# Optimization experiments

Measured on AMD Instinct MI355X. Metric: run time of the kernel, lower is better.

The kernel has to match this reference:

```python
import jax, jax.numpy as jnp
import numpy as np

NEG_INF = -1e30  # masked_softmax fill (squad util convention)


def setup_inputs() -> dict:
    key = jax.random.key(0)
    ks = jax.random.split(key, 5)
    B, S, H = 4, 2048, 512
    x = jax.random.normal(ks[0], (B, S, H), dtype=jnp.float32)
    mask = jax.random.randint(ks[1], (B, S), 0, 2, dtype=jnp.int32)
    mask = mask.at[:, 0].set(1)  # ensure at least one valid key per row
    W_comb = jax.random.normal(ks[2], (H, 3 * H), dtype=jnp.float32) * (1.0 / np.sqrt(H))
    b_comb = jnp.zeros((3 * H,), dtype=jnp.float32)
    W_out = jax.random.normal(ks[3], (H, H), dtype=jnp.float32) * (1.0 / np.sqrt(H))
    b_out = jnp.zeros((H,), dtype=jnp.float32)
    return {"x": x, "mask": mask, "W_comb": W_comb, "b_comb": b_comb,
            "W_out": W_out, "b_out": b_out}


def reference(x, mask, W_comb, b_comb, W_out, b_out):
    B, S, H = x.shape
    n_head = 8
    d = H // n_head
    scale = d ** 0.5
    qkv = x @ W_comb + b_comb                      # [B,S,3H]
    q, k, v = jnp.split(qkv, 3, axis=-1)
    q = q.reshape(B, S, n_head, d)
    k = k.reshape(B, S, n_head, d)
    v = v.reshape(B, S, n_head, d)
    # [B,h,Sq,Sk] scores; mask applies along the key axis
    scores = jnp.einsum('bqhd,bkhd->bhqk', q / scale, k)
    key_mask = (mask > 0)[:, None, None, :]        # [B,1,1,Sk]
    logits = jnp.where(key_mask, scores, NEG_INF)
    attn = jax.nn.softmax(logits, axis=-1)         # dropout = identity (eval)
    out = jnp.einsum('bhqk,bkhd->bqhd', attn, v).reshape(B, S, H)
    return out @ W_out + b_out
```

## Files before the change

kernel.cpp:

```cpp
#include <hip/hip_runtime.h>
#include <hip/hip_bf16.h>
#include <stdint.h>

typedef unsigned short u16;
typedef __attribute__((ext_vector_type(8))) __bf16 bf16x8;
typedef __attribute__((ext_vector_type(8))) unsigned short us8;
typedef __attribute__((ext_vector_type(4))) unsigned short us4;
typedef __attribute__((ext_vector_type(4))) float f32x4;
typedef __attribute__((ext_vector_type(16))) float f32x16;

#define KSCALE_Q 0.18033688011112042f

__device__ inline u16 f2bf(float f) {
  union { __bf16 b; u16 s; } x; x.b = (__bf16)f; return x.s;
}
__device__ inline f32x16 zero16() {
  f32x16 z; for (int i = 0; i < 16; ++i) z[i] = 0.f; return z;
}
__device__ __forceinline__ void gl_lds16(const u16* g, u16* l) {
  __builtin_amdgcn_global_load_lds(
      (const __attribute__((address_space(1))) void*)g,
      (__attribute__((address_space(3))) void*)l, 16, 0, 0);
}

__global__ __launch_bounds__(256) void prep(
    const float* __restrict__ x, const float* __restrict__ Wc,
    const float* __restrict__ Wo, const int* __restrict__ mask,
    u16* __restrict__ xbf, u16* __restrict__ wct, u16* __restrict__ wot,
    int* __restrict__ idx, int* __restrict__ nbv) {
  int r = blockIdx.x, tid = threadIdx.x;
  if (r < 4096) {
    int i = r * 256 + tid;
    float4 v = ((const float4*)x)[i];
    us4 o;
    o[0] = f2bf(v.x); o[1] = f2bf(v.y); o[2] = f2bf(v.z); o[3] = f2bf(v.w);
    ((us4*)xbf)[i] = o;
    return;
  }
  __shared__ float tile[32][33];
  __shared__ int ps[256];
  if (r < 5120) {
    const float* in; u16* outT; int R, C, bi;
    if (r < 4864) { in = Wc; outT = wct; R = 512; C = 1536; bi = r - 4096; }
    else          { in = Wo; outT = wot; R = 512; C = 512;  bi = r - 4864; }
    int nbx = C >> 5;
    int bx = bi % nbx, by = bi / nbx;
    int xq = tid & 31, yq = tid >> 5;
    int c0 = bx * 32, r0 = by * 32;
    for (int j = 0; j < 32; j += 8)
      tile[yq + j][xq] = in[(size_t)(r0 + yq + j) * C + c0 + xq];
    __syncthreads();
    for (int j = 0; j < 32; j += 8)
      outT[(size_t)(c0 + yq + j) * R + r0 + xq] = f2bf(tile[xq][yq + j]);
    return;
  }
  int b = r - 5120;
  const int* mrow = mask + b * 2048;
  int4 a = ((const int4*)mrow)[tid * 2];
  int4 c = ((const int4*)mrow)[tid * 2 + 1];
  int v[8] = {a.x, a.y, a.z, a.w, c.x, c.y, c.z, c.w};
  int cnt = 0;
  for (int i = 0; i < 8; ++i) cnt += (v[i] > 0);
  ps[tid] = cnt;
  __syncthreads();
  for (int off = 1; off < 256; off <<= 1) {
    int xv = ps[tid];
    int yv = (tid >= off) ? ps[tid - off] : 0;
    __syncthreads();
    ps[tid] = xv + yv;
    __syncthreads();
  }
  int total = ps[255];
  int pos = ps[tid] - cnt;
  int* ip = idx + b * 2048;
  for (int i = 0; i < 8; ++i)
    if (v[i] > 0) ip[pos++] = tid * 8 + i;
  for (int i = 0; i < 8; ++i) {
    int j = tid * 8 + i;
    if (j >= total) ip[j] = 0;
  }
  if (tid == 0) nbv[b] = total;
}

template <int OB>
__global__ __launch_bounds__(256) void gemm64(
    const u16* __restrict__ A, const u16* __restrict__ Bt,
    const float* __restrict__ bias, void* __restrict__ Cout,
    int N, int K, float oscale) {
  int m0 = blockIdx.y * 128, n0 = blockIdx.x * 64;
  __shared__ __align__(16) u16 As[128 * 32];
  __shared__ __align__(16) u16 Bs[64 * 32];
  int tid = threadIdx.x, wave = tid >> 6, lane = tid & 63;
  int quad = lane >> 4, l16 = lane & 15;
  int wm = (wave >> 1) * 64, wn = (wave & 1) * 32;

  int arow0 = wave * 32 + (lane >> 2);
  int acb = (lane & 3) ^ ((lane >> 3) & 3);
  const u16* ag0 = A + (size_t)(m0 + arow0) * K + acb * 8;
  const u16* ag1 = ag0 + (size_t)16 * K;
  u16* al0 = As + wave * 32 * 32;
  u16* al1 = al0 + 16 * 32;
  int brow = wave * 16 + (lane >> 2);
  const u16* bg = Bt + (size_t)(n0 + brow) * K + acb * 8;
  u16* bl = Bs + wave * 16 * 32;

  f32x4 acc[4][2];
  for (int i = 0; i < 4; ++i)
    for (int j = 0; j < 2; ++j) acc[i][j] = (f32x4){0.f, 0.f, 0.f, 0.f};

  int swz = (l16 >> 1) & 3;
  for (int kk = 0; kk < K; kk += 32) {
    __syncthreads();
    gl_lds16(ag0 + kk, al0);
    gl_lds16(ag1 + kk, al1);
    gl_lds16(bg + kk, bl);
    __syncthreads();
    bf16x8 af[4], bfr[2];
    for (int i = 0; i < 4; ++i)
      af[i] = *(const bf16x8*)(As + (wm + i * 16 + l16) * 32 +
                               (quad ^ swz) * 8);
    for (int j = 0; j < 2; ++j)
      bfr[j] = *(const bf16x8*)(Bs + (wn + j * 16 + l16) * 32 +
                                (quad ^ swz) * 8);
    for (int i = 0; i < 4; ++i)
      for (int j = 0; j < 2; ++j)
        acc[i][j] = __builtin_amdgcn_mfma_f32_16x16x32_bf16(
            af[i], bfr[j], acc[i][j], 0, 0, 0);
  }
  for (int j = 0; j < 2; ++j) {
    int col = n0 + wn + j * 16 + l16;
    float bv = bias[col];
    for (int i = 0; i < 4; ++i) {
      int rowb = m0 + wm + i * 16 + quad * 4;
      for (int rr = 0; rr < 4; ++rr) {
        float v = (acc[i][j][rr] + bv) * oscale;
        if (OB)
          ((u16*)Cout)[(size_t)(rowb + rr) * N + col] = f2bf(v);
        else
          ((float*)Cout)[(size_t)(rowb + rr) * N + col] = v;
      }
    }
  }
}

__global__ __launch_bounds__(256) void gemm_kv(
    const u16* __restrict__ A, const u16* __restrict__ Bt,
    const float* __restrict__ bias, u16* __restrict__ Kc,
    u16* __restrict__ VTc, const int* __restrict__ idx,
    const int* __restrict__ nbv) {
  const int K = 512, N = 1024;
  int b = blockIdx.z;
  int m0 = blockIdx.y * 128, n0 = blockIdx.x * 64;
  int npad = (nbv[b] + 127) & ~127;
  if (m0 >= npad) return;
  __shared__ __align__(16) u16 As[128 * 32];
  __shared__ __align__(16) u16 Bs[64 * 32];
  int tid = threadIdx.x, wave = tid >> 6, lane = tid & 63;
  int quad = lane >> 4, l16 = lane & 15;
  int wm = (wave >> 1) * 64, wn = (wave & 1) * 32;

  int arow0 = wave * 32 + (lane >> 2);
  int acb = (lane & 3) ^ ((lane >> 3) & 3);
  int g0 = idx[b * 2048 + m0 + arow0];
  int g1 = idx[b * 2048 + m0 + arow0 + 16];
  const u16* ag0 = A + ((size_t)(b * 2048 + g0)) * K + acb * 8;
  const u16* ag1 = A + ((size_t)(b * 2048 + g1)) * K + acb * 8;
  u16* al0 = As + wave * 32 * 32;
  u16* al1 = al0 + 16 * 32;
  int brow = wave * 16 + (lane >> 2);
  const u16* bg = Bt + (size_t)(n0 + brow) * K + acb * 8;
  u16* bl = Bs + wave * 16 * 32;

  f32x4 acc[4][2];
  for (int i = 0; i < 4; ++i)
    for (int j = 0; j < 2; ++j) acc[i][j] = (f32x4){0.f, 0.f, 0.f, 0.f};

  int swz = (l16 >> 1) & 3;
  for (int kk = 0; kk < K; kk += 32) {
    __syncthreads();
    gl_lds16(ag0 + kk, al0);
    gl_lds16(ag1 + kk, al1);
    gl_lds16(bg + kk, bl);
    __syncthreads();
    bf16x8 af[4], bfr[2];
    for (int i = 0; i < 4; ++i)
      af[i] = *(const bf16x8*)(As + (wm + i * 16 + l16) * 32 +
                               (quad ^ swz) * 8);
    for (int j = 0; j < 2; ++j)
      bfr[j] = *(const bf16x8*)(Bs + (wn + j * 16 + l16) * 32 +
                                (quad ^ swz) * 8);
    for (int i = 0; i < 4; ++i)
      for (int j = 0; j < 2; ++j)
        acc[i][j] = __builtin_amdgcn_mfma_f32_16x16x32_bf16(
            af[i], bfr[j], acc[i][j], 0, 0, 0);
  }
  for (int j = 0; j < 2; ++j) {
    int col = n0 + wn + j * 16 + l16;
    float bv = bias[col];
    if (col < 512) {
      for (int i = 0; i < 4; ++i) {
        int key0 = m0 + wm + i * 16 + quad * 4;
        for (int rr = 0; rr < 4; ++rr)
          Kc[((size_t)b * 2048 + key0 + rr) * 512 + col] =
              f2bf(acc[i][j][rr] + bv);
      }
    } else {
      int hd = col - 512;
      int h = hd >> 6, d = hd & 63;
      u16* vrow = VTc + ((size_t)(b * 8 + h) * 64 + d) * 2048;
      for (int i = 0; i < 4; ++i) {
        int key0 = m0 + wm + i * 16 + quad * 4;
        us4 pk;
        for (int rr = 0; rr < 4; ++rr) pk[rr] = f2bf(acc[i][j][rr] + bv);
        *(us4*)(vrow + key0) = pk;
      }
    }
  }
}

__global__ __launch_bounds__(256) void attn_kernel(
    const u16* __restrict__ Qc, const u16* __restrict__ Kc,
    const u16* __restrict__ VTc, const int* __restrict__ nbv,
    u16* __restrict__ aout) {
  int b = blockIdx.z, h = blockIdx.y, q0 = blockIdx.x * 128;
  int bh = b * 8 + h;
  int tid = threadIdx.x, wave = tid >> 6, lane = tid & 63;
  int l5 = lane & 31, hi = lane >> 5;
  int nb = nbv[b];
  int npad = (nb + 127) & ~127;

  __shared__ __align__(16) u16 Kt[128 * 64];
  __shared__ __align__(16) u16 Vt[64 * 128];
  __shared__ __align__(16) u16 Pw[4][32 * 136];

  int qrow = b * 2048 + q0 + wave * 32 + l5;
  bf16x8 qf[4];
  for (int s = 0; s < 4; ++s)
    qf[s] = *(const bf16x8*)(Qc + (size_t)qrow * 512 + h * 64 + s * 16 + hi * 8);

  f32x16 o[2];
  o[0] = zero16(); o[1] = zero16();
  float lsum = 0.f;

  int krr = lane >> 3;
  int kcb = (lane & 7) ^ krr;
  const u16* kg = Kc + ((size_t)(b * 2048) + wave * 32 + krr) * 512 + h * 64 +
                  kcb * 8;
  u16* kl = Kt + (wave * 32) * 64 + lane * 8;
  int vrr = lane >> 4;
  const u16* vg = VTc + ((size_t)(bh * 64) + wave * 16 + vrr) * 2048;
  u16* vl = Vt + (wave * 16) * 128 + lane * 8;

  u16* pw = &Pw[wave][0] + l5 * 136;

  for (int kt0 = 0; kt0 < npad; kt0 += 128) {
    __syncthreads();
    for (int i = 0; i < 4; ++i)
      gl_lds16(kg + (size_t)(kt0 + i * 8) * 512, kl + i * 8 * 64);
    for (int i = 0; i < 4; ++i) {
      int vcb = (lane & 15) ^ ((i * 4 + vrr) & 7);
      gl_lds16(vg + (size_t)(i * 4) * 2048 + kt0 + vcb * 8, vl + i * 4 * 128);
    }
    __syncthreads();

    for (int kg4 = 0; kg4 < 4; ++kg4) {
      int krow = kg4 * 32 + l5;
      const u16* kro = Kt + krow * 64;
      int rx = krow & 7;
      f32x16 sa = zero16();
      for (int s = 0; s < 4; ++s) {
        bf16x8 ka = *(const bf16x8*)(kro + ((s * 2 + hi) ^ rx) * 8);
        sa = __builtin_amdgcn_mfma_f32_32x32x16_bf16(ka, qf[s], sa, 0, 0, 0);
      }
      if (kt0 + 128 > nb) {
        for (int r = 0; r < 16; ++r) {
          int jg = kt0 + kg4 * 32 + (r & 3) + 8 * (r >> 2) + 4 * hi;
          if (jg >= nb) sa[r] = -1e30f;
        }
      }
      for (int mI = 0; mI < 4; ++mI) {
        us4 pk;
        for (int r = 0; r < 4; ++r) {
          float e = exp2f(sa[mI * 4 + r]);
          lsum += e;
          pk[r] = f2bf(e);
        }
        *(us4*)(pw + kg4 * 32 + mI * 8 + hi * 4) = pk;
      }
    }

    for (int kh = 0; kh < 2; ++kh)
      for (int t = 0; t < 4; ++t) {
        bf16x8 pb = *(const bf16x8*)(pw + kh * 64 + t * 16 + hi * 8);
        for (int dc = 0; dc < 2; ++dc) {
          int vrow = dc * 32 + l5;
          bf16x8 va = *(const bf16x8*)(
              Vt + vrow * 128 + ((kh * 8 + t * 2 + hi) ^ (vrow & 7)) * 8);
          o[dc] = __builtin_amdgcn_mfma_f32_32x32x16_bf16(va, pb, o[dc], 0, 0, 0);
        }
      }
  }

  lsum += __shfl_xor(lsum, 32);
  float inv = 1.f / lsum;
  for (int dc = 0; dc < 2; ++dc)
    for (int mI = 0; mI < 4; ++mI) {
      us4 pk;
      for (int r = 0; r < 4; ++r) pk[r] = f2bf(o[dc][mI * 4 + r] * inv);
      *(us4*)(aout + (size_t)qrow * 512 + h * 64 + dc * 32 + mI * 8 + hi * 4) =
          pk;
    }
}

extern "C" void kernel_launch(void* const* d_in, const int* in_sizes, int n_in,
                              void* d_out, int out_size, void* d_ws,
                              size_t ws_size, hipStream_t stream) {
  const float* x = (const float*)d_in[0];
  const int* mask = (const int*)d_in[1];
  const float* Wc = (const float*)d_in[2];
  const float* bc = (const float*)d_in[3];
  const float* Wo = (const float*)d_in[4];
  const float* bo = (const float*)d_in[5];
  float* out = (float*)d_out;

  char* ws = (char*)d_ws;
  u16* xbf = (u16*)(ws);
  u16* wct = (u16*)(ws + 8388608);
  u16* wot = (u16*)(ws + 9961472);
  u16* Qc  = (u16*)(ws + 10485760);
  u16* Kc  = (u16*)(ws + 18874368);
  u16* vtc = (u16*)(ws + 27262976);
  int* idx = (int*)(ws + 35651584);
  int* nbv = (int*)(ws + 35684352);
  u16* aout = xbf;

  prep<<<5124, 256, 0, stream>>>(x, Wc, Wo, mask, xbf, wct, wot, idx, nbv);
  gemm64<1><<<dim3(8, 64), 256, 0, stream>>>(
      xbf, wct, bc, Qc, 512, 512, KSCALE_Q);
  gemm_kv<<<dim3(16, 16, 4), 256, 0, stream>>>(
      xbf, wct + (size_t)512 * 512, bc + 512, Kc, vtc, idx, nbv);
  attn_kernel<<<dim3(16, 8, 4), 256, 0, stream>>>(Qc, Kc, vtc, nbv, aout);
  gemm64<0><<<dim3(8, 64), 256, 0, stream>>>(
      aout, wot, bo, out, 512, 512, 1.0f);
}
```

Measured before the change: 168.4 us.

## Deepen GEMM K tile to 64 and keep attention P in registers via permlane swap

Both GEMM kernels now stage 64-wide K slices per barrier pair instead of 32, halving the number of sync rounds and using an 8-way XOR swizzle. The attention kernel drops the per-wave LDS buffer for the softmax probabilities. It repacks the exp results into MFMA B-operand layout in registers using permlane32 swaps, and the V tile swizzle is widened to 16 to match. The intent is to cut LDS round-trips and barriers, at the cost of more LDS per GEMM block and reliance on the permlane builtin, with a shuffle fallback.

```diff
diff --git a/kernel.cpp b/kernel.cpp
--- a/kernel.cpp
+++ b/kernel.cpp
@@ -3,16 +3,22 @@
 #include <stdint.h>
 
 typedef unsigned short u16;
+typedef unsigned int u32;
 typedef __attribute__((ext_vector_type(8))) __bf16 bf16x8;
 typedef __attribute__((ext_vector_type(8))) unsigned short us8;
 typedef __attribute__((ext_vector_type(4))) unsigned short us4;
 typedef __attribute__((ext_vector_type(4))) float f32x4;
 typedef __attribute__((ext_vector_type(16))) float f32x16;
+typedef __attribute__((ext_vector_type(4))) unsigned int u32x4;
+typedef __attribute__((ext_vector_type(2))) unsigned int u32x2;
 
 #define KSCALE_Q 0.18033688011112042f
 
 __device__ inline u16 f2bf(float f) {
   union { __bf16 b; u16 s; } x; x.b = (__bf16)f; return x.s;
+}
+__device__ inline u32 packbf(float a, float b) {
+  return (u32)f2bf(a) | ((u32)f2bf(b) << 16);
 }
 __device__ inline f32x16 zero16() {
   f32x16 z; for (int i = 0; i < 16; ++i) z[i] = 0.f; return z;
@@ -21,6 +27,19 @@
   __builtin_amdgcn_global_load_lds(
       (const __attribute__((address_space(1))) void*)g,
       (__attribute__((address_space(3))) void*)l, 16, 0, 0);
+}
+__device__ __forceinline__ void pl32swap(u32& a, u32& b) {
+#if __has_builtin(__builtin_amdgcn_permlane32_swap)
+  u32x2 r = __builtin_amdgcn_permlane32_swap(a, b, false, false);
+  a = r[0]; b = r[1];
+#else
+  u32 ta = (u32)__shfl_xor((int)a, 32);
+  u32 tb = (u32)__shfl_xor((int)b, 32);
+  int hi = (threadIdx.x & 63) >> 5;
+  u32 na = hi ? tb : a;
+  u32 nb = hi ? b : ta;
+  a = na; b = nb;
+#endif
 }
 
 __global__ __launch_bounds__(256) void prep(
@@ -88,44 +107,43 @@
     const float* __restrict__ bias, void* __restrict__ Cout,
     int N, int K, float oscale) {
   int m0 = blockIdx.y * 128, n0 = blockIdx.x * 64;
-  __shared__ __align__(16) u16 As[128 * 32];
-  __shared__ __align__(16) u16 Bs[64 * 32];
+  __shared__ __align__(16) u16 As[128 * 64];
+  __shared__ __align__(16) u16 Bs[64 * 64];
   int tid = threadIdx.x, wave = tid >> 6, lane = tid & 63;
   int quad = lane >> 4, l16 = lane & 15;
   int wm = (wave >> 1) * 64, wn = (wave & 1) * 32;
 
-  int arow0 = wave * 32 + (lane >> 2);
-  int acb = (lane & 3) ^ ((lane >> 3) & 3);
-  const u16* ag0 = A + (size_t)(m0 + arow0) * K + acb * 8;
-  const u16* ag1 = ag0 + (size_t)16 * K;
-  u16* al0 = As + wave * 32 * 32;
-  u16* al1 = al0 + 16 * 32;
-  int brow = wave * 16 + (lane >> 2);
-  const u16* bg = Bt + (size_t)(n0 + brow) * K + acb * 8;
-  u16* bl = Bs + wave * 16 * 32;
+  int r8 = lane >> 3;
+  int cb = (lane & 7) ^ r8;
+  const u16* ag = A + (size_t)(m0 + wave * 32 + r8) * K + cb * 8;
+  const u16* bg = Bt + (size_t)(n0 + wave * 16 + r8) * K + cb * 8;
+  u16* al = As + (wave * 32) * 64 + lane * 8;
+  u16* bl = Bs + (wave * 16) * 64 + lane * 8;
 
   f32x4 acc[4][2];
   for (int i = 0; i < 4; ++i)
     for (int j = 0; j < 2; ++j) acc[i][j] = (f32x4){0.f, 0.f, 0.f, 0.f};
 
-  int swz = (l16 >> 1) & 3;
-  for (int kk = 0; kk < K; kk += 32) {
-    __syncthreads();
-    gl_lds16(ag0 + kk, al0);
-    gl_lds16(ag1 + kk, al1);
-    gl_lds16(bg + kk, bl);
-    __syncthreads();
-    bf16x8 af[4], bfr[2];
+  int rx = l16 & 7;
+  for (int kk = 0; kk < K; kk += 64) {
+    __syncthreads();
     for (int i = 0; i < 4; ++i)
-      af[i] = *(const bf16x8*)(As + (wm + i * 16 + l16) * 32 +
-                               (quad ^ swz) * 8);
-    for (int j = 0; j < 2; ++j)
-      bfr[j] = *(const bf16x8*)(Bs + (wn + j * 16 + l16) * 32 +
-                                (quad ^ swz) * 8);
-    for (int i = 0; i < 4; ++i)
+      gl_lds16(ag + kk + (size_t)(i * 8) * K, al + i * 8 * 64);
+    for (int i = 0; i < 2; ++i)
+      gl_lds16(bg + kk + (size_t)(i * 8) * K, bl + i * 8 * 64);
+    __syncthreads();
+    for (int ks = 0; ks < 2; ++ks) {
+      int pos = ((ks * 4 + quad) ^ rx) * 8;
+      bf16x8 af[4], bfr[2];
+      for (int i = 0; i < 4; ++i)
+        af[i] = *(const bf16x8*)(As + (wm + i * 16 + l16) * 64 + pos);
       for (int j = 0; j < 2; ++j)
-        acc[i][j] = __builtin_amdgcn_mfma_f32_16x16x32_bf16(
-            af[i], bfr[j], acc[i][j], 0, 0, 0);
+        bfr[j] = *(const bf16x8*)(Bs + (wn + j * 16 + l16) * 64 + pos);
+      for (int i = 0; i < 4; ++i)
+        for (int j = 0; j < 2; ++j)
+          acc[i][j] = __builtin_amdgcn_mfma_f32_16x16x32_bf16(
+              af[i], bfr[j], acc[i][j], 0, 0, 0);
+    }
   }
   for (int j = 0; j < 2; ++j) {
     int col = n0 + wn + j * 16 + l16;
@@ -153,46 +171,47 @@
   int m0 = blockIdx.y * 128, n0 = blockIdx.x * 64;
   int npad = (nbv[b] + 127) & ~127;
   if (m0 >= npad) return;
-  __shared__ __align__(16) u16 As[128 * 32];
-  __shared__ __align__(16) u16 Bs[64 * 32];
+  __shared__ __align__(16) u16 As[128 * 64];
+  __shared__ __align__(16) u16 Bs[64 * 64];
   int tid = threadIdx.x, wave = tid >> 6, lane = tid & 63;
   int quad = lane >> 4, l16 = lane & 15;
   int wm = (wave >> 1) * 64, wn = (wave & 1) * 32;
 
-  int arow0 = wave * 32 + (lane >> 2);
-  int acb = (lane & 3) ^ ((lane >> 3) & 3);
-  int g0 = idx[b * 2048 + m0 + arow0];
-  int g1 = idx[b * 2048 + m0 + arow0 + 16];
-  const u16* ag0 = A + ((size_t)(b * 2048 + g0)) * K + acb * 8;
-  const u16* ag1 = A + ((size_t)(b * 2048 + g1)) * K + acb * 8;
-  u16* al0 = As + wave * 32 * 32;
-  u16* al1 = al0 + 16 * 32;
-  int brow = wave * 16 + (lane >> 2);
-  const u16* bg = Bt + (size_t)(n0 + brow) * K + acb * 8;
-  u16* bl = Bs + wave * 16 * 32;
+  int r8 = lane >> 3;
+  int cb = (lane & 7) ^ r8;
+  const u16* agp[4];
+  for (int i = 0; i < 4; ++i) {
+    int gi = idx[b * 2048 + m0 + wave * 32 + i * 8 + r8];
+    agp[i] = A + (size_t)(b * 2048 + gi) * K + cb * 8;
+  }
+  const u16* bg = Bt + (size_t)(n0 + wave * 16 + r8) * K + cb * 8;
+  u16* al = As + (wave * 32) * 64 + lane * 8;
+  u16* bl = Bs + (wave * 16) * 64 + lane * 8;
 
   f32x4 acc[4][2];
   for (int i = 0; i < 4; ++i)
     for (int j = 0; j < 2; ++j) acc[i][j] = (f32x4){0.f, 0.f, 0.f, 0.f};
 
-  int swz = (l16 >> 1) & 3;
-  for (int kk = 0; kk < K; kk += 32) {
-    __syncthreads();
-    gl_lds16(ag0 + kk, al0);
-    gl_lds16(ag1 + kk, al1);
-    gl_lds16(bg + kk, bl);
-    __syncthreads();
-    bf16x8 af[4], bfr[2];
+  int rx = l16 & 7;
+  for (int kk = 0; kk < K; kk += 64) {
+    __syncthreads();
     for (int i = 0; i < 4; ++i)
-      af[i] = *(const bf16x8*)(As + (wm + i * 16 + l16) * 32 +
-                               (quad ^ swz) * 8);
-    for (int j = 0; j < 2; ++j)
-      bfr[j] = *(const bf16x8*)(Bs + (wn + j * 16 + l16) * 32 +
-                                (quad ^ swz) * 8);
-    for (int i = 0; i < 4; ++i)
+      gl_lds16(agp[i] + kk, al + i * 8 * 64);
+    for (int i = 0; i < 2; ++i)
+      gl_lds16(bg + kk + (size_t)(i * 8) * K, bl + i * 8 * 64);
+    __syncthreads();
+    for (int ks = 0; ks < 2; ++ks) {
+      int pos = ((ks * 4 + quad) ^ rx) * 8;
+      bf16x8 af[4], bfr[2];
+      for (int i = 0; i < 4; ++i)
+        af[i] = *(const bf16x8*)(As + (wm + i * 16 + l16) * 64 + pos);
       for (int j = 0; j < 2; ++j)
-        acc[i][j] = __builtin_amdgcn_mfma_f32_16x16x32_bf16(
-            af[i], bfr[j], acc[i][j], 0, 0, 0);
+        bfr[j] = *(const bf16x8*)(Bs + (wn + j * 16 + l16) * 64 + pos);
+      for (int i = 0; i < 4; ++i)
+        for (int j = 0; j < 2; ++j)
+          acc[i][j] = __builtin_amdgcn_mfma_f32_16x16x32_bf16(
+              af[i], bfr[j], acc[i][j], 0, 0, 0);
+    }
   }
   for (int j = 0; j < 2; ++j) {
     int col = n0 + wn + j * 16 + l16;
@@ -231,7 +250,6 @@
 
   __shared__ __align__(16) u16 Kt[128 * 64];
   __shared__ __align__(16) u16 Vt[64 * 128];
-  __shared__ __align__(16) u16 Pw[4][32 * 136];
 
   int qrow = b * 2048 + q0 + wave * 32 + l5;
   bf16x8 qf[4];
@@ -248,18 +266,17 @@
                   kcb * 8;
   u16* kl = Kt + (wave * 32) * 64 + lane * 8;
   int vrr = lane >> 4;
-  const u16* vg = VTc + ((size_t)(bh * 64) + wave * 16 + vrr) * 2048;
   u16* vl = Vt + (wave * 16) * 128 + lane * 8;
-
-  u16* pw = &Pw[wave][0] + l5 * 136;
 
   for (int kt0 = 0; kt0 < npad; kt0 += 128) {
     __syncthreads();
     for (int i = 0; i < 4; ++i)
       gl_lds16(kg + (size_t)(kt0 + i * 8) * 512, kl + i * 8 * 64);
     for (int i = 0; i < 4; ++i) {
-      int vcb = (lane & 15) ^ ((i * 4 + vrr) & 7);
-      gl_lds16(vg + (size_t)(i * 4) * 2048 + kt0 + vcb * 8, vl + i * 4 * 128);
+      int vr = wave * 16 + i * 4 + vrr;
+      int vcb = (lane & 15) ^ (vr & 15);
+      gl_lds16(VTc + ((size_t)(bh * 64) + vr) * 2048 + kt0 + vcb * 8,
+               vl + i * 4 * 128);
     }
     __syncthreads();
 
@@ -278,27 +295,30 @@
           if (jg >= nb) sa[r] = -1e30f;
         }
       }
-      for (int mI = 0; mI < 4; ++mI) {
-        us4 pk;
-        for (int r = 0; r < 4; ++r) {
-          float e = exp2f(sa[mI * 4 + r]);
-          lsum += e;
-          pk[r] = f2bf(e);
-        }
-        *(us4*)(pw + kg4 * 32 + mI * 8 + hi * 4) = pk;
-      }
-    }
-
-    for (int kh = 0; kh < 2; ++kh)
-      for (int t = 0; t < 4; ++t) {
-        bf16x8 pb = *(const bf16x8*)(pw + kh * 64 + t * 16 + hi * 8);
+      u32 pk[8];
+      for (int j = 0; j < 8; ++j) {
+        float e0 = __builtin_amdgcn_exp2f(sa[2 * j]);
+        float e1 = __builtin_amdgcn_exp2f(sa[2 * j + 1]);
+        lsum += e0 + e1;
+        pk[j] = packbf(e0, e1);
+      }
+      for (int t = 0; t < 2; ++t) {
+        u32 a0 = pk[t * 4 + 0], a2 = pk[t * 4 + 2];
+        u32 a1 = pk[t * 4 + 1], a3 = pk[t * 4 + 3];
+        pl32swap(a0, a2);
+        pl32swap(a1, a3);
+        u32x4 qv; qv[0] = a0; qv[1] = a1; qv[2] = a2; qv[3] = a3;
+        bf16x8 pb = __builtin_bit_cast(bf16x8, qv);
+        int cblk = kg4 * 4 + t * 2 + hi;
         for (int dc = 0; dc < 2; ++dc) {
           int vrow = dc * 32 + l5;
-          bf16x8 va = *(const bf16x8*)(
-              Vt + vrow * 128 + ((kh * 8 + t * 2 + hi) ^ (vrow & 7)) * 8);
-          o[dc] = __builtin_amdgcn_mfma_f32_32x32x16_bf16(va, pb, o[dc], 0, 0, 0);
+          bf16x8 va = *(const bf16x8*)(Vt + vrow * 128 +
+                                       ((cblk ^ (vrow & 15)) * 8));
+          o[dc] = __builtin_amdgcn_mfma_f32_32x32x16_bf16(va, pb, o[dc],
+                                                          0, 0, 0);
         }
       }
+    }
   }
 
   lsum += __shfl_xor(lsum, 32);
```

Result: faster. 159.0 us (-5.6%).
